# Kernel tuning notes

Measured on AMD Instinct MI355X. Metric: run time of the kernel, lower is better.

Reference implementation:

```python
import jax, jax.numpy as jnp
import numpy as np

K = 8
NUM_BLOCKS = 4
ALPHA = K / (K + 1)  # 8/9


def _knn_norm_adj(xyz, k):
    """xyz: (B, 3, N) -> symmetric-normalized GCN adjacency (B, N, N).

    Mirrors knn_point(k, xyz, xyz) -> indices[:, 1:] -> get_adjacency_matrix,
    then the (input-independent) DenseGCNConv normalization: self loops set to 1,
    deg clamped >= 1, D^-1/2 A D^-1/2. adj is identical for every GCN call, so
    it is normalized once here.
    """
    x2 = jnp.sum(xyz * xyz, axis=1)                       # (B, N)
    inner = jnp.einsum('bci,bcj->bij', xyz, xyz)          # (B, N, N)
    dist = x2[:, :, None] + x2[:, None, :] - 2.0 * inner  # squared pairwise dist
    _, idx = jax.lax.top_k(-dist, k)                      # (B, N, k); self (dist 0) first
    nbr = idx[:, :, 1:]                                   # drop self -> k-1 neighbors
    B, N = x2.shape
    adj = jnp.zeros((B, N, N), xyz.dtype)
    adj = adj.at[jnp.arange(B)[:, None, None],
                 jnp.arange(N)[None, :, None], nbr].set(1.0)
    ar = jnp.arange(N)
    adj = adj.at[:, ar, ar].set(1.0)                      # add_loop=True
    dis = jnp.clip(jnp.sum(adj, axis=-1), 1.0, None) ** -0.5  # (B, N)
    return dis[:, :, None] * adj * dis[:, None, :]


def setup_inputs() -> dict:
    key = jax.random.key(0)
    ks = jax.random.split(key, 6)
    B, N, C = 16, 2048, 128
    s = 1.0 / np.sqrt(C).astype(np.float32)
    return {
        'xyz': jax.random.normal(ks[0], (B, 3, N), jnp.float32),
        'points': jax.random.normal(ks[1], (B, C, N), jnp.float32),
        'Wc': jax.random.normal(ks[2], (4, C, C), jnp.float32) * s,   # nn.Linear weights (out,in)
        'Wg': jax.random.normal(ks[3], (4, C, C), jnp.float32) * s,   # DenseGCNConv lin weights
        'Wuc': jax.random.normal(ks[4], (6, C), jnp.float32) * s,
        'Wug': jax.random.normal(ks[5], (6, C), jnp.float32) * s,
    }


def reference(xyz, points, Wc, Wg, Wuc, Wug):
    adj = _knn_norm_adj(xyz, K)                 # (B, N, N)
    pts = jnp.swapaxes(points, 1, 2)            # (B, N, C) channel-last internally
    for i in range(NUM_BLOCKS):
        shortcut = pts
        act = jax.nn.relu(pts)
        center = jnp.einsum('bnc,dc->bnd', act, Wc[i])                 # Linear on relu(points)
        grouped = adj @ jnp.einsum('bnc,dc->bnd', shortcut, Wg[i])     # DenseGCNConv on shortcut
        pts = (1.0 - ALPHA) * grouped + ALPHA * center + shortcut
    # unpool head
    points_xyz = jnp.einsum('bnd,od->bno', pts, Wuc)                   # (B, N, 6)
    grouped_xyz = adj @ jnp.einsum('bnd,od->bno', pts, Wug)            # (B, N, 6)
    new = ALPHA * points_xyz + (1.0 - ALPHA) * grouped_xyz
    B, N, _ = new.shape
    new = jnp.swapaxes(new, 1, 2).reshape(B, 3, 2, N) + xyz[:, :, None, :]
    new_xyz = new.reshape(B, 3, 2 * N)
    return new_xyz, jnp.swapaxes(pts, 1, 2)     # ((B,3,2N), (B,C,N))
```

## Files before the change

### kernel.cpp

```cpp
#include <hip/hip_runtime.h>
#include <hip/hip_bf16.h>

static constexpr int NB = 16;
static constexpr int NP = 2048;
static constexpr int NC = 128;
#define ALPHA_F ((float)(8.0/9.0))
#define OMA_F   ((float)(1.0 - 8.0/9.0))

typedef __attribute__((ext_vector_type(8))) short bfrag;
typedef __attribute__((ext_vector_type(4))) float ffrag;

union BU { bfrag v; uint4 u; unsigned int w[4]; };

__device__ inline void split2(float x, float y, unsigned& hi, unsigned& lo) {
    __hip_bfloat162 h = __float22bfloat162_rn(make_float2(x, y));
    float2 hb = __bfloat1622float2(h);
    __hip_bfloat162 l = __float22bfloat162_rn(make_float2(x - hb.x, y - hb.y));
    __builtin_memcpy(&hi, &h, 4);
    __builtin_memcpy(&lo, &l, 4);
}

__device__ inline void split1(float x, unsigned short& h, unsigned short& l) {
    __hip_bfloat16 hb = __float2bfloat16(x);
    float hf = __bfloat162float(hb);
    __hip_bfloat16 lb = __float2bfloat16(x - hf);
    __builtin_memcpy(&h, &hb, 2);
    __builtin_memcpy(&l, &lb, 2);
}

__global__ __launch_bounds__(256) void knn_kernel(const float* __restrict__ xyz,
                                                  int* __restrict__ nbr) {
    __shared__ float4 sp[NP];
    __shared__ float  md[64][33];
    __shared__ int    mi[64][33];
    int b = blockIdx.y;
    const float* X = xyz + (size_t)b * 3 * NP;
    for (int m = threadIdx.x; m < NP; m += 256) {
        float x = X[m], y = X[NP + m], z = X[2 * NP + m];
        sp[m] = make_float4(x, y, z, x * x + y * y + z * z);
    }
    __syncthreads();

    int tid = threadIdx.x;
    int p = tid >> 2;
    int q = tid & 3;
    int base = blockIdx.x * 64;
    int n = base + p;
    float4 me = sp[n];
    float xi = me.x, yi = me.y, zi = me.z, qi = me.w;

    float gd[8]; int gi[8];
#pragma unroll
    for (int t = 0; t < 8; ++t) { gd[t] = 3.4e38f; gi[t] = 0; }
#pragma unroll 1
    for (int g = 0; g < 64; ++g) {
        float gm = 3.4e38f;
#pragma unroll
        for (int i = 0; i < 8; ++i) {
            int j = (g * 8 + i) * 4 + q;
            float4 c4v = sp[j];
            float inner = xi * c4v.x + yi * c4v.y + zi * c4v.z;
            float d = qi + c4v.w - 2.0f * inner;
            gm = fminf(gm, d);
        }
        bool c[8];
#pragma unroll
        for (int t = 0; t < 8; ++t) c[t] = gm < gd[t];
#pragma unroll
        for (int t = 7; t >= 1; --t) {
            gd[t] = c[t - 1] ? gd[t - 1] : (c[t] ? gm : gd[t]);
            gi[t] = c[t - 1] ? gi[t - 1] : (c[t] ? g : gi[t]);
        }
        gd[0] = c[0] ? gm : gd[0];
        gi[0] = c[0] ? g : gi[0];
    }

    unsigned long long mask = 0ull;
#pragma unroll
    for (int t = 0; t < 8; ++t) mask |= (1ull << gi[t]);

    float bd[8]; int bi[8];
#pragma unroll
    for (int t = 0; t < 8; ++t) { bd[t] = 3.4e38f; bi[t] = 0; }
    while (mask) {
        int g = (int)__builtin_ctzll(mask);
        mask &= (mask - 1ull);
#pragma unroll
        for (int i = 0; i < 8; ++i) {
            int j = (g * 8 + i) * 4 + q;
            float4 c4v = sp[j];
            float inner = xi * c4v.x + yi * c4v.y + zi * c4v.z;
            float d = qi + c4v.w - 2.0f * inner;
            bool c[8];
#pragma unroll
            for (int t = 0; t < 8; ++t) c[t] = d < bd[t];
#pragma unroll
            for (int t = 7; t >= 1; --t) {
                bd[t] = c[t - 1] ? bd[t - 1] : (c[t] ? d : bd[t]);
                bi[t] = c[t - 1] ? bi[t - 1] : (c[t] ? j : bi[t]);
            }
            bd[0] = c[0] ? d : bd[0];
            bi[0] = c[0] ? j : bi[0];
        }
    }
#pragma unroll
    for (int t = 0; t < 8; ++t) {
        md[p][q * 8 + t] = bd[t];
        mi[p][q * 8 + t] = bi[t];
    }
    __syncthreads();

    if (tid < 64) {
        float fd[8]; int fi[8];
#pragma unroll
        for (int t = 0; t < 8; ++t) { fd[t] = 3.4e38f; fi[t] = 0; }
#pragma unroll 4
        for (int cc = 0; cc < 32; ++cc) {
            float d = md[tid][cc];
            int j = mi[tid][cc];
            bool c[8];
#pragma unroll
            for (int t = 0; t < 8; ++t) c[t] = d < fd[t];
#pragma unroll
            for (int t = 7; t >= 1; --t) {
                fd[t] = c[t - 1] ? fd[t - 1] : (c[t] ? d : fd[t]);
                fi[t] = c[t - 1] ? fi[t - 1] : (c[t] ? j : fi[t]);
            }
            fd[0] = c[0] ? d : fd[0];
            fi[0] = c[0] ? j : fi[0];
        }
        int row = b * NP + base + tid;
#pragma unroll
        for (int t = 0; t < 7; ++t) nbr[row * 7 + t] = fi[t + 1];
    }
}

__global__ __launch_bounds__(256) void transpose_kernel(const float* __restrict__ in,
                                                        float* __restrict__ out,
                                                        int R, int S) {
    __shared__ float t[32][33];
    int b = blockIdx.z;
    int s0 = blockIdx.x * 32, r0 = blockIdx.y * 32;
    const float* I = in + (size_t)b * R * S;
    float* O = out + (size_t)b * R * S;
#pragma unroll
    for (int i = 0; i < 4; ++i) {
        int r = r0 + threadIdx.y + i * 8;
        t[threadIdx.y + i * 8][threadIdx.x] = I[(size_t)r * S + s0 + threadIdx.x];
    }
    __syncthreads();
#pragma unroll
    for (int i = 0; i < 4; ++i) {
        int s = s0 + threadIdx.y + i * 8;
        O[(size_t)s * R + r0 + threadIdx.x] = t[threadIdx.x][threadIdx.y + i * 8];
    }
}

__global__ __launch_bounds__(256) void prep_w_kernel(const float* __restrict__ Wc,
                                                     const float* __restrict__ Wg,
                                                     uint4* __restrict__ WP) {
    int t = blockIdx.x * 256 + threadIdx.x;
    int ncol = t & 127;
    int quad = (t >> 7) & 3;
    int s = (t >> 9) & 3;
    int mat = (t >> 11) & 1;
    int layer = t >> 12;
    const float* W = (mat ? Wg : Wc) + (size_t)layer * NC * NC + (size_t)ncol * NC + s * 32 + quad * 8;
    float4 a = *((const float4*)W);
    float4 b = *((const float4*)(W + 4));
    BU hi, lo;
    split2(a.x, a.y, hi.w[0], lo.w[0]);
    split2(a.z, a.w, hi.w[1], lo.w[1]);
    split2(b.x, b.y, hi.w[2], lo.w[2]);
    split2(b.z, b.w, hi.w[3], lo.w[3]);
    WP[t * 2] = hi.u;
    WP[t * 2 + 1] = lo.u;
}

template <int MODE>
__global__ __launch_bounds__(512) void gemm_fused_kernel(const float* __restrict__ Asrc,
                                                         const float* __restrict__ Y2in,
                                                         const int* __restrict__ nbr,
                                                         const uint4* __restrict__ WPc,
                                                         const uint4* __restrict__ WPg,
                                                         float* __restrict__ Zout,
                                                         float* __restrict__ Y2out) {
    __shared__ unsigned short AhT[64][136];
    __shared__ unsigned short AlT[64][136];
    __shared__ int s_nb[448];
    int tid = threadIdx.x;
    int wid = tid >> 6, lane = tid & 63;
    int quad = lane >> 4, l15 = lane & 15;
    int xcd = blockIdx.x & 7;
    int slot = blockIdx.x >> 3;
    int bb = xcd * 2 + (slot >> 5);
    int n0 = (slot & 31) << 6;
    size_t m0 = (size_t)bb * NP + n0;
    int ncol = wid * 16 + l15;

    BU Bch[4], Bcl[4], Bgh[4], Bgl[4];
#pragma unroll
    for (int s = 0; s < 4; ++s) {
        int idx = ((s * 4 + quad) * 128 + ncol) * 2;
        Bch[s].u = WPc[idx];
        Bcl[s].u = WPc[idx + 1];
        Bgh[s].u = WPg[idx];
        Bgl[s].u = WPg[idx + 1];
    }

    if (MODE == 1) {
        if (tid < 448) s_nb[tid] = nbr[m0 * 7 + tid];
        __syncthreads();
        size_t bbase = (size_t)bb * NP;
#pragma unroll 1
        for (int it = 0; it < 4; ++it) {
            int f = tid + it * 512;
            int r = f >> 5, c4 = (f & 31) * 4;
            size_t row = m0 + r;
            float4 z = *((const float4*)(Asrc + row * NC + c4));
            float4 acc = *((const float4*)(Y2in + row * NC + c4));
#pragma unroll
            for (int t = 0; t < 7; ++t) {
                int j = s_nb[r * 7 + t];
                float4 v = *((const float4*)(Y2in + (bbase + (size_t)j) * NC + c4));
                acc.x += v.x; acc.y += v.y; acc.z += v.z; acc.w += v.w;
            }
            float4 a;
            a.x = OMA_F * (0.125f * acc.x) + z.x;
            a.y = OMA_F * (0.125f * acc.y) + z.y;
            a.z = OMA_F * (0.125f * acc.z) + z.z;
            a.w = OMA_F * (0.125f * acc.w) + z.w;
            unsigned h01, l01, h23, l23;
            split2(a.x, a.y, h01, l01);
            split2(a.z, a.w, h23, l23);
            *((uint2*)&AhT[r][c4]) = make_uint2(h01, h23);
            *((uint2*)&AlT[r][c4]) = make_uint2(l01, l23);
        }
    } else {
#pragma unroll
        for (int it = 0; it < 4; ++it) {
            int f = tid + it * 512;
            int c = f >> 4, rq = (f & 15) * 4;
            float4 v = *((const float4*)(Asrc + ((size_t)bb * NC + c) * NP + n0 + rq));
            float vv[4] = {v.x, v.y, v.z, v.w};
#pragma unroll
            for (int k = 0; k < 4; ++k) {
                unsigned short h, l;
                split1(vv[k], h, l);
                AhT[rq + k][c] = h;
                AlT[rq + k][c] = l;
            }
        }
    }
    __syncthreads();

    ffrag accC[4], accG[4];
#pragma unroll
    for (int mt = 0; mt < 4; ++mt) { accC[mt] = (ffrag)0.0f; accG[mt] = (ffrag)0.0f; }

#pragma unroll
    for (int s = 0; s < 4; ++s) {
#pragma unroll
        for (int mt = 0; mt < 4; ++mt) {
            int m = mt * 16 + l15;
            int k = s * 32 + quad * 8;
            BU ah, al, rh, rl;
            ah.u = *((const uint4*)&AhT[m][k]);
            al.u = *((const uint4*)&AlT[m][k]);
#pragma unroll
            for (int w = 0; w < 4; ++w) {
                unsigned msk = ((ah.w[w] & 0x80008000u) >> 15) * 0xFFFFu;
                rh.w[w] = ah.w[w] & ~msk;
                rl.w[w] = al.w[w] & ~msk;
            }
            accC[mt] = __builtin_amdgcn_mfma_f32_16x16x32_bf16(rh.v, Bch[s].v, accC[mt], 0, 0, 0);
            accC[mt] = __builtin_amdgcn_mfma_f32_16x16x32_bf16(rh.v, Bcl[s].v, accC[mt], 0, 0, 0);
            accC[mt] = __builtin_amdgcn_mfma_f32_16x16x32_bf16(rl.v, Bch[s].v, accC[mt], 0, 0, 0);
            accG[mt] = __builtin_amdgcn_mfma_f32_16x16x32_bf16(ah.v, Bgh[s].v, accG[mt], 0, 0, 0);
            accG[mt] = __builtin_amdgcn_mfma_f32_16x16x32_bf16(ah.v, Bgl[s].v, accG[mt], 0, 0, 0);
            accG[mt] = __builtin_amdgcn_mfma_f32_16x16x32_bf16(al.v, Bgh[s].v, accG[mt], 0, 0, 0);
        }
    }

#pragma unroll
    for (int mt = 0; mt < 4; ++mt) {
        int rbase = mt * 16 + quad * 4;
#pragma unroll
        for (int r = 0; r < 4; ++r) {
            int rr = rbase + r;
            unsigned hb = ((unsigned)AhT[rr][ncol]) << 16;
            unsigned lb = ((unsigned)AlT[rr][ncol]) << 16;
            float hp, lp;
            __builtin_memcpy(&hp, &hb, 4);
            __builtin_memcpy(&lp, &lb, 4);
            float p = hp + lp;
            size_t idx = (m0 + rr) * NC + ncol;
            Zout[idx] = p + ALPHA_F * accC[mt][r];
            Y2out[idx] = accG[mt][r];
        }
    }
}

__global__ __launch_bounds__(256) void agg_kernel(const float* __restrict__ Z,
                                                  const float* __restrict__ Y2,
                                                  const int* __restrict__ nbr,
                                                  float* __restrict__ Pout) {
    int tid = threadIdx.x;
    int lane = tid & 31, rl = tid >> 5;
    int xcd = blockIdx.x & 7;
    int slot = blockIdx.x >> 3;
    int bb = xcd * 2 + (slot >> 8);
    int rblk = slot & 255;
    size_t row = ((size_t)bb << 11) + rblk * 8 + rl;
    const int* nb = nbr + row * 7;
    size_t off = row * NC + lane * 4;
    float4 ys = *((const float4*)(Y2 + off));
    size_t bbase = (size_t)bb * NP * NC;
#pragma unroll
    for (int t = 0; t < 7; ++t) {
        int j = nb[t];
        float4 v = *((const float4*)(Y2 + bbase + (size_t)j * NC + lane * 4));
        ys.x += v.x; ys.y += v.y; ys.z += v.z; ys.w += v.w;
    }
    float4 z = *((const float4*)(Z + off));
    float4 o;
    o.x = OMA_F * (0.125f * ys.x) + z.x;
    o.y = OMA_F * (0.125f * ys.y) + z.y;
    o.z = OMA_F * (0.125f * ys.z) + z.z;
    o.w = OMA_F * (0.125f * ys.w) + z.w;
    *((float4*)(Pout + off)) = o;
}

__global__ __launch_bounds__(256) void final_gemm_kernel(const float* __restrict__ P,
                                                         const float* __restrict__ Wuc,
                                                         const float* __restrict__ Wug,
                                                         float* __restrict__ U) {
    __shared__ float s1[6 * NC], s2[6 * NC];
    for (int m = threadIdx.x; m < 6 * NC; m += 256) { s1[m] = Wuc[m]; s2[m] = Wug[m]; }
    __syncthreads();
    size_t row = (size_t)blockIdx.x * 256 + threadIdx.x;
    const float4* prow = (const float4*)(P + row * NC);
    float a1[6] = {0, 0, 0, 0, 0, 0}, a2[6] = {0, 0, 0, 0, 0, 0};
#pragma unroll 4
    for (int c4 = 0; c4 < NC / 4; ++c4) {
        float4 p = prow[c4];
#pragma unroll
        for (int o = 0; o < 6; ++o) {
            float4 w1 = *((const float4*)&s1[o * NC + c4 * 4]);
            float4 w2 = *((const float4*)&s2[o * NC + c4 * 4]);
            a1[o] += p.x * w1.x + p.y * w1.y + p.z * w1.z + p.w * w1.w;
            a2[o] += p.x * w2.x + p.y * w2.y + p.z * w2.z + p.w * w2.w;
        }
    }
#pragma unroll
    for (int o = 0; o < 6; ++o) {
        U[row * 12 + o] = a1[o];
        U[row * 12 + 6 + o] = a2[o];
    }
}

__global__ __launch_bounds__(256) void final_out_kernel(const float* __restrict__ U,
                                                        const int* __restrict__ nbr,
                                                        const float* __restrict__ xyz,
                                                        float* __restrict__ out) {
    size_t row = (size_t)blockIdx.x * 256 + threadIdx.x;
    int b = (int)(row >> 11), n = (int)(row & 2047);
    const int* nb = nbr + row * 7;
    float u1[6], u2[6];
#pragma unroll
    for (int o = 0; o < 6; ++o) { u1[o] = U[row * 12 + o]; u2[o] = U[row * 12 + 6 + o]; }
#pragma unroll
    for (int t = 0; t < 7; ++t) {
        int j = nb[t];
        const float* Uj = U + ((size_t)b * NP + j) * 12 + 6;
#pragma unroll
        for (int o = 0; o < 6; ++o) u2[o] += Uj[o];
    }
#pragma unroll
    for (int c = 0; c < 3; ++c)
#pragma unroll
        for (int s = 0; s < 2; ++s) {
            int o = c * 2 + s;
            float val = ALPHA_F * u1[o] + OMA_F * (0.125f * u2[o])
                      + xyz[(size_t)b * 3 * NP + (size_t)c * NP + n];
            out[(size_t)b * 3 * 2 * NP + (size_t)c * 2 * NP + (size_t)s * NP + n] = val;
        }
}

extern "C" void kernel_launch(void* const* d_in, const int* in_sizes, int n_in,
                              void* d_out, int out_size, void* d_ws, size_t ws_size,
                              hipStream_t stream) {
    const float* xyz    = (const float*)d_in[0];
    const float* points = (const float*)d_in[1];
    const float* Wc     = (const float*)d_in[2];
    const float* Wg     = (const float*)d_in[3];
    const float* Wuc    = (const float*)d_in[4];
    const float* Wug    = (const float*)d_in[5];
    float* out = (float*)d_out;

    char* ws = (char*)d_ws;
    size_t o = 0;
    int* nbr  = (int*)(ws + o);     o += (size_t)NB * NP * 7 * 4;
    uint4* WP = (uint4*)(ws + o);   o += (size_t)32768 * 16;
    float* Za = (float*)(ws + o);   o += (size_t)NB * NP * NC * 4;
    float* Ya = (float*)(ws + o);   o += (size_t)NB * NP * NC * 4;
    float* Zb = (float*)(ws + o);   o += (size_t)NB * NP * NC * 4;
    float* Yb = (float*)(ws + o);   o += (size_t)NB * NP * NC * 4;
    float* U  = (float*)(ws + o);   o += (size_t)NB * NP * 12 * 4;

    const int GEMM_GRID = NB * NP / 64;
    #define WPC(L) (WP + (size_t)((L) * 2 + 0) * 4096)
    #define WPG(L) (WP + (size_t)((L) * 2 + 1) * 4096)

    prep_w_kernel<<<64, 256, 0, stream>>>(Wc, Wg, WP);
    knn_kernel<<<dim3(NP / 64, NB), 256, 0, stream>>>(xyz, nbr);
    gemm_fused_kernel<0><<<GEMM_GRID, 512, 0, stream>>>(points, nullptr, nullptr,
        WPC(0), WPG(0), Za, Ya);
    gemm_fused_kernel<1><<<GEMM_GRID, 512, 0, stream>>>(Za, Ya, nbr,
        WPC(1), WPG(1), Zb, Yb);
    gemm_fused_kernel<1><<<GEMM_GRID, 512, 0, stream>>>(Zb, Yb, nbr,
        WPC(2), WPG(2), Za, Ya);
    gemm_fused_kernel<1><<<GEMM_GRID, 512, 0, stream>>>(Za, Ya, nbr,
        WPC(3), WPG(3), Zb, Yb);
    float* P5 = Za;
    agg_kernel<<<dim3(NB * NP / 8), 256, 0, stream>>>(Zb, Yb, nbr, P5);
    final_gemm_kernel<<<dim3(NB * NP / 256), 256, 0, stream>>>(P5, Wuc, Wug, U);
    final_out_kernel<<<dim3(NB * NP / 256), 256, 0, stream>>>(U, nbr, xyz, out);
    transpose_kernel<<<dim3(NC / 32, NP / 32, NB), dim3(32, 8), 0, stream>>>(
        P5, out + (size_t)NB * 3 * 2 * NP, NP, NC);
}
```

Before: 228.8 us.

## Split KNN candidate scan across eight lanes per point with swizzled LDS

The KNN kernel now uses 512 threads per block, with eight lanes per query point instead of four. Each lane scans 32 groups of 8 candidates instead of 64. The point table in shared memory is XOR-swizzled to avoid bank conflicts under the new access pattern. The shared buffer is reused for the per-lane partial top-8 lists, which adds a barrier before reuse and doubles the serial final merge per point (64 candidates instead of 32). Coarse group pruning is now per 8 groups of 8 per lane, so each lane can rescan up to 8 selected groups, and the higher thread count changes occupancy.

```diff
diff --git a/kernel.cpp b/kernel.cpp
--- a/kernel.cpp
+++ b/kernel.cpp
@@ -28,37 +28,39 @@
     __builtin_memcpy(&l, &lb, 2);
 }
 
-__global__ __launch_bounds__(256) void knn_kernel(const float* __restrict__ xyz,
+__global__ __launch_bounds__(512) void knn_kernel(const float* __restrict__ xyz,
                                                   int* __restrict__ nbr) {
-    __shared__ float4 sp[NP];
-    __shared__ float  md[64][33];
-    __shared__ int    mi[64][33];
+    __shared__ __align__(16) char shraw[33280];
+    float4* sp = (float4*)shraw;
+    float (*md)[65] = (float(*)[65])shraw;
+    int   (*mi)[65] = (int(*)[65])(shraw + 64 * 65 * sizeof(float));
+
+    int tid = threadIdx.x;
     int b = blockIdx.y;
     const float* X = xyz + (size_t)b * 3 * NP;
-    for (int m = threadIdx.x; m < NP; m += 256) {
+    for (int m = tid; m < NP; m += 512) {
         float x = X[m], y = X[NP + m], z = X[2 * NP + m];
-        sp[m] = make_float4(x, y, z, x * x + y * y + z * z);
-    }
-    __syncthreads();
-
-    int tid = threadIdx.x;
-    int p = tid >> 2;
-    int q = tid & 3;
+        sp[m ^ ((m >> 6) & 7)] = make_float4(x, y, z, x * x + y * y + z * z);
+    }
+    __syncthreads();
+
+    int p = tid >> 3;
+    int q = tid & 7;
     int base = blockIdx.x * 64;
     int n = base + p;
-    float4 me = sp[n];
+    float4 me = sp[n ^ ((n >> 6) & 7)];
     float xi = me.x, yi = me.y, zi = me.z, qi = me.w;
 
     float gd[8]; int gi[8];
 #pragma unroll
     for (int t = 0; t < 8; ++t) { gd[t] = 3.4e38f; gi[t] = 0; }
 #pragma unroll 1
-    for (int g = 0; g < 64; ++g) {
+    for (int g = 0; g < 32; ++g) {
         float gm = 3.4e38f;
+        int jb = (g * 64 + q) ^ (g & 7);
 #pragma unroll
         for (int i = 0; i < 8; ++i) {
-            int j = (g * 8 + i) * 4 + q;
-            float4 c4v = sp[j];
+            float4 c4v = sp[jb + i * 8];
             float inner = xi * c4v.x + yi * c4v.y + zi * c4v.z;
             float d = qi + c4v.w - 2.0f * inner;
             gm = fminf(gm, d);
@@ -75,20 +77,22 @@
         gi[0] = c[0] ? g : gi[0];
     }
 
-    unsigned long long mask = 0ull;
-#pragma unroll
-    for (int t = 0; t < 8; ++t) mask |= (1ull << gi[t]);
+    unsigned mask = 0u;
+#pragma unroll
+    for (int t = 0; t < 8; ++t) mask |= (1u << gi[t]);
 
     float bd[8]; int bi[8];
 #pragma unroll
     for (int t = 0; t < 8; ++t) { bd[t] = 3.4e38f; bi[t] = 0; }
     while (mask) {
-        int g = (int)__builtin_ctzll(mask);
-        mask &= (mask - 1ull);
+        int g = (int)__builtin_ctz(mask);
+        mask &= (mask - 1u);
+        int sw = g & 7;
+        int jb = g * 64 + q;
 #pragma unroll
         for (int i = 0; i < 8; ++i) {
-            int j = (g * 8 + i) * 4 + q;
-            float4 c4v = sp[j];
+            int j0 = jb + i * 8;
+            float4 c4v = sp[j0 ^ sw];
             float inner = xi * c4v.x + yi * c4v.y + zi * c4v.z;
             float d = qi + c4v.w - 2.0f * inner;
             bool c[8];
@@ -97,12 +101,13 @@
 #pragma unroll
             for (int t = 7; t >= 1; --t) {
                 bd[t] = c[t - 1] ? bd[t - 1] : (c[t] ? d : bd[t]);
-                bi[t] = c[t - 1] ? bi[t - 1] : (c[t] ? j : bi[t]);
+                bi[t] = c[t - 1] ? bi[t - 1] : (c[t] ? j0 : bi[t]);
             }
             bd[0] = c[0] ? d : bd[0];
-            bi[0] = c[0] ? j : bi[0];
-        }
-    }
+            bi[0] = c[0] ? j0 : bi[0];
+        }
+    }
+    __syncthreads();
 #pragma unroll
     for (int t = 0; t < 8; ++t) {
         md[p][q * 8 + t] = bd[t];
@@ -115,7 +120,7 @@
 #pragma unroll
         for (int t = 0; t < 8; ++t) { fd[t] = 3.4e38f; fi[t] = 0; }
 #pragma unroll 4
-        for (int cc = 0; cc < 32; ++cc) {
+        for (int cc = 0; cc < 64; ++cc) {
             float d = md[tid][cc];
             int j = mi[tid][cc];
             bool c[8];
@@ -413,7 +418,7 @@
     #define WPG(L) (WP + (size_t)((L) * 2 + 1) * 4096)
 
     prep_w_kernel<<<64, 256, 0, stream>>>(Wc, Wg, WP);
-    knn_kernel<<<dim3(NP / 64, NB), 256, 0, stream>>>(xyz, nbr);
+    knn_kernel<<<dim3(NP / 64, NB), 512, 0, stream>>>(xyz, nbr);
     gemm_fused_kernel<0><<<GEMM_GRID, 512, 0, stream>>>(points, nullptr, nullptr,
         WPC(0), WPG(0), Za, Ya);
     gemm_fused_kernel<1><<<GEMM_GRID, 512, 0, stream>>>(Za, Ya, nbr,
```

New measurement: 241.6 us. 5.6% more time.

## Restructure kNN coarse pass with contiguous groups, packed keys and shuffle merge

Applied to the files above, without the earlier changes.

Candidate grouping in the kNN kernel changes from interleaved groups of 8 to contiguous groups of 32 points, and each lane scans 16 of them. The group minimum distance and group index are packed into one unsigned key so a single-array insertion sort is used. The four lanes' top-8 group lists are then merged with xor shuffles and a bitonic network. Shared-memory points get an XOR swizzle to avoid bank conflicts. The changes aim to cut LDS traffic and compare/select work in the coarse pass, at the risk of tie or precision differences from truncating the low distance bits and clamping at zero.

```diff
diff --git a/kernel.cpp b/kernel.cpp
--- a/kernel.cpp
+++ b/kernel.cpp
@@ -37,7 +37,7 @@
     const float* X = xyz + (size_t)b * 3 * NP;
     for (int m = threadIdx.x; m < NP; m += 256) {
         float x = X[m], y = X[NP + m], z = X[2 * NP + m];
-        sp[m] = make_float4(x, y, z, x * x + y * y + z * z);
+        sp[m ^ ((m >> 5) & 7)] = make_float4(x, y, z, x * x + y * y + z * z);
     }
     __syncthreads();
 
@@ -46,38 +46,57 @@
     int q = tid & 3;
     int base = blockIdx.x * 64;
     int n = base + p;
-    float4 me = sp[n];
+    float4 me = sp[n ^ ((n >> 5) & 7)];
     float xi = me.x, yi = me.y, zi = me.z, qi = me.w;
 
-    float gd[8]; int gi[8];
-#pragma unroll
-    for (int t = 0; t < 8; ++t) { gd[t] = 3.4e38f; gi[t] = 0; }
+    unsigned gd[8];
+#pragma unroll
+    for (int t = 0; t < 8; ++t) gd[t] = 0x7F7FFFFFu;
 #pragma unroll 1
-    for (int g = 0; g < 64; ++g) {
-        float gm = 3.4e38f;
-#pragma unroll
-        for (int i = 0; i < 8; ++i) {
-            int j = (g * 8 + i) * 4 + q;
-            float4 c4v = sp[j];
-            float inner = xi * c4v.x + yi * c4v.y + zi * c4v.z;
-            float d = qi + c4v.w - 2.0f * inner;
-            gm = fminf(gm, d);
-        }
+    for (int gg = 0; gg < 16; ++gg) {
+        int g = q * 16 + gg;
+        const float4* gp = sp + g * 32;
+        float m0 = 3.4e38f, m1 = m0, m2 = m0, m3 = m0;
+#pragma unroll
+        for (int k = 0; k < 32; k += 4) {
+            float4 a0 = gp[k], a1 = gp[k + 1], a2 = gp[k + 2], a3 = gp[k + 3];
+            m0 = fminf(m0, qi + a0.w - 2.0f * (xi * a0.x + yi * a0.y + zi * a0.z));
+            m1 = fminf(m1, qi + a1.w - 2.0f * (xi * a1.x + yi * a1.y + zi * a1.z));
+            m2 = fminf(m2, qi + a2.w - 2.0f * (xi * a2.x + yi * a2.y + zi * a2.z));
+            m3 = fminf(m3, qi + a3.w - 2.0f * (xi * a3.x + yi * a3.y + zi * a3.z));
+        }
+        float gm = fmaxf(fminf(fminf(m0, m1), fminf(m2, m3)), 0.0f);
+        unsigned pg; __builtin_memcpy(&pg, &gm, 4);
+        pg = (pg & ~63u) | (unsigned)g;
         bool c[8];
 #pragma unroll
-        for (int t = 0; t < 8; ++t) c[t] = gm < gd[t];
-#pragma unroll
-        for (int t = 7; t >= 1; --t) {
-            gd[t] = c[t - 1] ? gd[t - 1] : (c[t] ? gm : gd[t]);
-            gi[t] = c[t - 1] ? gi[t - 1] : (c[t] ? g : gi[t]);
-        }
-        gd[0] = c[0] ? gm : gd[0];
-        gi[0] = c[0] ? g : gi[0];
-    }
-
+        for (int t = 0; t < 8; ++t) c[t] = pg < gd[t];
+#pragma unroll
+        for (int t = 7; t >= 1; --t)
+            gd[t] = c[t - 1] ? gd[t - 1] : (c[t] ? pg : gd[t]);
+        gd[0] = c[0] ? pg : gd[0];
+    }
+
+#define CEU(A, B) { unsigned _lo = (A) < (B) ? (A) : (B); \
+                    unsigned _hi = (A) < (B) ? (B) : (A); (A) = _lo; (B) = _hi; }
+    unsigned cA[8];
+#pragma unroll
+    for (int i = 0; i < 8; ++i) {
+        unsigned pb = (unsigned)__shfl_xor((int)gd[7 - i], 1);
+        cA[i] = gd[i] < pb ? gd[i] : pb;
+    }
+    CEU(cA[0], cA[4]); CEU(cA[1], cA[5]); CEU(cA[2], cA[6]); CEU(cA[3], cA[7]);
+    CEU(cA[0], cA[2]); CEU(cA[1], cA[3]); CEU(cA[4], cA[6]); CEU(cA[5], cA[7]);
+    CEU(cA[0], cA[1]); CEU(cA[2], cA[3]); CEU(cA[4], cA[5]); CEU(cA[6], cA[7]);
+    unsigned dA[8];
+#pragma unroll
+    for (int i = 0; i < 8; ++i) {
+        unsigned pb = (unsigned)__shfl_xor((int)cA[7 - i], 2);
+        dA[i] = cA[i] < pb ? cA[i] : pb;
+    }
     unsigned long long mask = 0ull;
 #pragma unroll
-    for (int t = 0; t < 8; ++t) mask |= (1ull << gi[t]);
+    for (int i = 0; i < 8; ++i) mask |= (1ull << (dA[i] & 63u));
 
     float bd[8]; int bi[8];
 #pragma unroll
@@ -85,10 +104,12 @@
     while (mask) {
         int g = (int)__builtin_ctzll(mask);
         mask &= (mask - 1ull);
+        int sw = g & 7;
+        int jb = g * 32 + q;
 #pragma unroll
         for (int i = 0; i < 8; ++i) {
-            int j = (g * 8 + i) * 4 + q;
-            float4 c4v = sp[j];
+            int j0 = jb + i * 4;
+            float4 c4v = sp[j0 ^ sw];
             float inner = xi * c4v.x + yi * c4v.y + zi * c4v.z;
             float d = qi + c4v.w - 2.0f * inner;
             bool c[8];
@@ -97,10 +118,10 @@
 #pragma unroll
             for (int t = 7; t >= 1; --t) {
                 bd[t] = c[t - 1] ? bd[t - 1] : (c[t] ? d : bd[t]);
-                bi[t] = c[t - 1] ? bi[t - 1] : (c[t] ? j : bi[t]);
+                bi[t] = c[t - 1] ? bi[t - 1] : (c[t] ? j0 : bi[t]);
             }
             bd[0] = c[0] ? d : bd[0];
-            bi[0] = c[0] ? j : bi[0];
+            bi[0] = c[0] ? j0 : bi[0];
         }
     }
 #pragma unroll
```

After: 232.4 us. Within noise of the previous version (+1.6%).
